# Kernel tuning notes

Hardware: AMD Instinct MI355X
Metric: run time of the kernel (lower is better)

## Reference

```python
import jax, jax.numpy as jnp
import numpy as np

B, T, D, NH, C = 64, 256, 768, 12, 7
DH = D // NH

def setup_inputs() -> dict:
    key = jax.random.key(0)
    ks = jax.random.split(key, 8)
    s = 0.02
    H = jax.random.normal(ks[0], (B, T, D), jnp.float32)
    num_turns = jax.random.randint(ks[1], (B,), 1, T + 1)  # >=1 real turn each
    Wq = jax.random.normal(ks[2], (D, D), jnp.float32) * s
    Wk = jax.random.normal(ks[3], (D, D), jnp.float32) * s
    Wv = jax.random.normal(ks[4], (D, D), jnp.float32) * s
    Wo = jax.random.normal(ks[5], (D, D), jnp.float32) * s
    Wc = jax.random.normal(ks[6], (2 * D, C), jnp.float32) * s
    bq = jnp.zeros((D,), jnp.float32); bk = jnp.zeros((D,), jnp.float32)
    bv = jnp.zeros((D,), jnp.float32); bo = jnp.zeros((D,), jnp.float32)
    bc = jnp.zeros((C,), jnp.float32)
    return dict(H=H, Wq=Wq, bq=bq, Wk=Wk, bk=bk, Wv=Wv, bv=bv, Wo=Wo, bo=bo,
                Wc=Wc, bc=bc, num_turns=num_turns)

def reference(H, Wq, bq, Wk, bk, Wv, bv, Wo, bo, Wc, bc, num_turns):
    # Vectorized form of the per-(dialogue, turn) python loop:
    # turn t attends (multi-head) over strictly-earlier real turns.
    q = (H @ Wq + bq).reshape(B, T, NH, DH)
    k = (H @ Wk + bk).reshape(B, T, NH, DH)
    v = (H @ Wv + bv).reshape(B, T, NH, DH)
    scores = jnp.einsum('bqhd,bkhd->bhqk', q, k) / np.sqrt(DH).astype(np.float32)
    tq = jnp.arange(T)
    # strict causal (key < query) AND key is a real (non-padding) turn
    mask = (tq[None, :, None] > tq[None, None, :]) & (tq[None, None, :] < num_turns[:, None, None])  # [B,T,T]
    scores = jnp.where(mask[:, None], scores, -1e30)
    attn = jax.nn.softmax(scores, axis=-1)
    row_valid = mask.any(-1)  # [B,T]; False for t=0 (and beyond padding prefix logic)
    attn = jnp.where(row_valid[:, None, :, None], attn, 0.0)
    ctx = jnp.einsum('bhqk,bkhd->bqhd', attn, v).reshape(B, T, D)
    c = ctx @ Wo + bo
    # t==0: original sets c_t = exact zeros (no out-proj bias) -> zero full rows
    c = jnp.where(row_valid[:, :, None], c, 0.0)
    z = jnp.concatenate([H, c], axis=-1)          # [B,T,2D]
    all_logits = z @ Wc + bc                       # [B,T,C]
    final_logits = all_logits[jnp.arange(B), num_turns - 1]  # [B,C]
    return all_logits, final_logits
```

## Files before the change

kernel.cpp:

```cpp
#include <hip/hip_runtime.h>
#include <hip/hip_bf16.h>

#define B_  64
#define T_  256
#define D_  768
#define NH_ 12
#define DH_ 64
#define C_  7
#define QS_ 2304

using f32x4  = __attribute__((ext_vector_type(4))) float;
using bf16x8 = __attribute__((ext_vector_type(8))) __bf16;
using u16x8  = __attribute__((ext_vector_type(8))) unsigned short;
using u16x4  = __attribute__((ext_vector_type(4))) unsigned short;
using s16x4  = __attribute__((ext_vector_type(4))) short;

#if defined(__has_builtin)
#if __has_builtin(__builtin_amdgcn_mfma_f32_16x16x16bf16_1k)
#define HAS_MFMA16 1
#endif
#endif

static __device__ inline unsigned short f2bf(float f) {
    union { float f; unsigned u; } c; c.f = f;
    unsigned u = c.u;
    return (unsigned short)((u + 0x7fffu + ((u >> 16) & 1u)) >> 16);
}

#define ASYNC16(gp, lp) __builtin_amdgcn_global_load_lds(                      \
    (const __attribute__((address_space(1))) unsigned int*)(gp),               \
    (__attribute__((address_space(3))) unsigned int*)(lp), 16, 0, 0)

#define PRO_CONV 6144
#define PRO_TR   1728
#define PRO_BIAS 9
#define PRO_WF   13
#define PRO_ALL  (PRO_CONV + PRO_TR + PRO_BIAS + PRO_WF)

__global__ __launch_bounds__(256) void prologue(
    const float* __restrict__ H, unsigned short* __restrict__ Hb,
    const float* __restrict__ Wq, const float* __restrict__ Wk,
    const float* __restrict__ Wv,
    unsigned short* __restrict__ Wqkvt,
    const float* __restrict__ bq, const float* __restrict__ bk,
    const float* __restrict__ bv, float* __restrict__ bqkv,
    const float* __restrict__ Wo, const float* __restrict__ Wc,
    const float* __restrict__ bo,
    float* __restrict__ Wf, float* __restrict__ boc)
{
    __shared__ float tile[32][33];
    __shared__ float wcs[D_ * C_];
    const int blk = blockIdx.x;
    const int tid = threadIdx.x;

    if (blk < PRO_CONV) {
        const int i = (blk * 256 + tid) * 8;
        float4 f0 = *(const float4*)(H + i);
        float4 f1 = *(const float4*)(H + i + 4);
        u16x8 u;
        u[0] = f2bf(f0.x); u[1] = f2bf(f0.y); u[2] = f2bf(f0.z); u[3] = f2bf(f0.w);
        u[4] = f2bf(f1.x); u[5] = f2bf(f1.y); u[6] = f2bf(f1.z); u[7] = f2bf(f1.w);
        *(uint4*)(Hb + i) = __builtin_bit_cast(uint4, u);
    } else if (blk < PRO_CONV + PRO_TR) {
        const int tb = blk - PRO_CONV;
        const int z = tb / 576;
        const int rem = tb - z * 576;
        const int bx = (rem % 24) * 32;
        const int by = (rem / 24) * 32;
        const size_t wsz = (size_t)D_ * D_;
        const float* W = (z == 0) ? Wq : (z == 1) ? Wk : Wv;
        unsigned short* Wt = Wqkvt + (size_t)z * wsz;
        const int tx = tid & 31;
        const int ty = tid >> 5;
#pragma unroll
        for (int i = ty; i < 32; i += 8)
            tile[i][tx] = W[(size_t)(by + i) * D_ + bx + tx];
        __syncthreads();
#pragma unroll
        for (int i = ty; i < 32; i += 8)
            Wt[(size_t)(bx + i) * D_ + by + tx] = f2bf(tile[tx][i]);
    } else if (blk < PRO_CONV + PRO_TR + PRO_BIAS) {
        const int i = (blk - PRO_CONV - PRO_TR) * 256 + tid;
        if (i < D_)          bqkv[i] = bq[i];
        else if (i < 2 * D_) bqkv[i] = bk[i - D_];
        else if (i < 3 * D_) bqkv[i] = bv[i - 2 * D_];
    } else {
        const int fb = blk - (PRO_CONV + PRO_TR + PRO_BIAS);
        for (int i = tid; i < D_ * C_; i += 256)
            wcs[i] = Wc[(size_t)D_ * C_ + i];
        __syncthreads();
        if (fb < 12) {
            const int dl = tid >> 2;
            const int ks = tid & 3;
            const int d  = fb * 64 + dl;
            const float* wrow = Wo + (size_t)d * D_;
            float a[C_] = {};
            for (int e = ks * 192; e < ks * 192 + 192; ++e) {
                const float w = wrow[e];
#pragma unroll
                for (int c = 0; c < C_; ++c) a[c] += w * wcs[e * C_ + c];
            }
#pragma unroll
            for (int c = 0; c < C_; ++c) {
                a[c] += __shfl_xor(a[c], 1, 64);
                a[c] += __shfl_xor(a[c], 2, 64);
            }
            if (ks == 0) {
#pragma unroll
                for (int c = 0; c < C_; ++c) Wf[d * C_ + c] = a[c];
            }
        } else if (tid < C_) {
            float a = 0.f;
            for (int e = 0; e < D_; ++e) a += bo[e] * wcs[e * C_ + tid];
            boc[tid] = a;
        }
    }
}

#define QBM 128
#define QBN 128
#define QBK 64
#define KQ  768
#define NKT 12

#define BAR   do { __builtin_amdgcn_s_barrier();                               \
                   __builtin_amdgcn_sched_barrier(0); } while (0)
#define VMW(n) do { asm volatile("s_waitcnt vmcnt(" #n ")" ::: "memory");      \
                    __builtin_amdgcn_sched_barrier(0); } while (0)

__global__ __launch_bounds__(256, 2) void gemm_qkv_db(
    const unsigned short* __restrict__ A,
    const unsigned short* __restrict__ Bt,
    const float* __restrict__ bias,
    unsigned short* __restrict__ qkvb,
    unsigned short* __restrict__ Vt,
    const int* __restrict__ num_turns)
{
    __shared__ unsigned short As[2][QBM * QBK];
    __shared__ unsigned short Bs[2][QBN * QBK];

    const int tid = threadIdx.x;
    const int wv  = tid >> 6;
    const int ln  = tid & 63;
    const int hi  = ln >> 4;
    const int lo  = ln & 15;
    const int wm  = (wv & 1) * 64;
    const int wn  = (wv >> 1) * 64;

    const int L   = blockIdx.y * gridDim.x + blockIdx.x;
    const int wg  = (L & 7) * 288 + (L >> 3);
    const int my  = wg / 18;
    const int nx  = wg - my * 18;

    const int row0 = my * QBM;
    const int col0 = nx * QBN;

    if (col0 >= D_ && (row0 & (T_ - 1)) != 0) {
        if (num_turns[row0 >> 8] <= 128) return;
    }

    const int s0 = tid >> 3;
    const int ch = (tid & 7) ^ (s0 & 7);
    const unsigned short* a0 = A  + (size_t)(row0 + s0) * KQ + ch * 8;
    const unsigned short* b0 = Bt + (size_t)(col0 + s0) * KQ + ch * 8;

#define STG(t, q) do {                                                         \
    _Pragma("unroll") for (int c = 0; c < 4; ++c) {                            \
        ASYNC16(a0 + (size_t)(t) * QBK + (size_t)c * 32 * KQ,                  \
                &As[q][c * 2048 + wv * 512]);                                  \
        ASYNC16(b0 + (size_t)(t) * QBK + (size_t)c * 32 * KQ,                  \
                &Bs[q][c * 2048 + wv * 512]);                                  \
    }                                                                          \
} while (0)

    const int fcs[2] = { (0 * 4 + hi) ^ (lo & 7), (1 * 4 + hi) ^ (lo & 7) };

    f32x4 acc[4][4] = {};

#define TILE(t, q, qn) do {                                                    \
    if ((t) + 1 < NKT) { STG((t) + 1, qn); VMW(8); }                           \
    else               { VMW(0); }                                             \
    BAR;                                                                       \
    _Pragma("unroll") for (int s = 0; s < 2; ++s) {                            \
        const int fc = fcs[s];                                                 \
        bf16x8 af[4], bfr[4];                                                  \
        _Pragma("unroll") for (int i = 0; i < 4; ++i)                          \
            af[i] = *(const bf16x8*)&As[q][(wm + i * 16 + lo) * QBK + fc * 8]; \
        _Pragma("unroll") for (int j = 0; j < 4; ++j)                          \
            bfr[j] = *(const bf16x8*)&Bs[q][(wn + j * 16 + lo) * QBK + fc * 8];\
        __builtin_amdgcn_s_setprio(1);                                         \
        _Pragma("unroll") for (int i = 0; i < 4; ++i)                          \
        _Pragma("unroll") for (int j = 0; j < 4; ++j)                          \
            acc[i][j] = __builtin_amdgcn_mfma_f32_16x16x32_bf16(               \
                af[i], bfr[j], acc[i][j], 0, 0, 0);                            \
        __builtin_amdgcn_s_setprio(0);                                         \
    }                                                                          \
    BAR;                                                                       \
} while (0)

    STG(0, 0);
#pragma unroll
    for (int g = 0; g < NKT; g += 2) {
        TILE(g + 0, 0, 1);
        TILE(g + 1, 1, 0);
    }
#undef STG
#undef TILE

    const int bidx = row0 >> 8;
    const int t0   = row0 & (T_ - 1);
    if (col0 >= 1536) {
#pragma unroll
        for (int j = 0; j < 4; ++j) {
            const int dcol = (col0 - 1536) + wn + j * 16 + lo;
            const float bcol = bias[col0 + wn + j * 16 + lo];
            unsigned short* vrow =
                Vt + ((size_t)(bidx * NH_ + (dcol >> 6)) * DH_ + (dcol & 63)) * T_ + t0;
#pragma unroll
            for (int i = 0; i < 4; ++i) {
                u16x4 pk;
#pragma unroll
                for (int r = 0; r < 4; ++r) pk[r] = f2bf(acc[i][j][r] + bcol);
                *(u16x4*)(vrow + wm + i * 16 + hi * 4) = pk;
            }
        }
        return;
    }
#pragma unroll
    for (int j = 0; j < 4; ++j) {
        const int col = col0 + wn + j * 16 + lo;
        const float bcol = bias[col];
#pragma unroll
        for (int i = 0; i < 4; ++i) {
#pragma unroll
            for (int r = 0; r < 4; ++r) {
                const int row = row0 + wm + i * 16 + hi * 4 + r;
                qkvb[(size_t)row * QS_ + col] = f2bf(acc[i][j][r] + bcol);
            }
        }
    }
}

#if HAS_MFMA16
__global__ __launch_bounds__(512) void attn_fused(
    const unsigned short* __restrict__ qkv, const unsigned short* __restrict__ Vt,
    const int* __restrict__ num_turns, unsigned short* __restrict__ ctx)
{
    __shared__ unsigned short Klds[256 * 64];
    __shared__ unsigned short Vlds[64 * 256];

    const int bh = blockIdx.x;
    const int b = bh / NH_;
    const int h = bh - b * NH_;
    const int tid = threadIdx.x;
    const int wave = tid >> 6;
    const int lane = tid & 63;
    const int hi = lane >> 4;
    const int lo = lane & 15;
    const int lo7 = lo & 7;

    const int nt = num_turns[b];
    const int kend16 = (min(254, nt - 1) >> 4) + 1;
    const int vst = (kend16 <= 8) ? 128 : 256;

    const unsigned short* qb  = qkv + (size_t)(b * T_) * QS_ + h * DH_;
    const unsigned short* kb  = qb + D_;
    const unsigned short* vtb = Vt + (size_t)bh * DH_ * T_;

    {
        const int nkc = kend16 * 128;
        for (int q = tid; q < nkc; q += 512) {
            const int row = q >> 3;
            const int c   = q & 7;
            const int sl  = c ^ (row & 7);
            uint4 v = *(const uint4*)(kb + (size_t)row * QS_ + c * 8);
            *(uint4*)&Klds[row * 64 + sl * 8] = v;
        }
    }
    if (vst == 256) {
        for (int q = tid; q < 2048; q += 512) {
            const int d  = q >> 5;
            const int c  = q & 31;
            const int sl = c ^ (d & 7);
            uint4 v = *(const uint4*)(vtb + (size_t)d * T_ + c * 8);
            *(uint4*)&Vlds[d * 256 + sl * 8] = v;
        }
    } else {
        for (int q = tid; q < 1024; q += 512) {
            const int d  = q >> 4;
            const int c  = q & 15;
            const int sl = c ^ (d & 7);
            uint4 v = *(const uint4*)(vtb + (size_t)d * T_ + c * 8);
            *(uint4*)&Vlds[d * 128 + sl * 8] = v;
        }
    }

    bf16x8 aqs[2][2];
#pragma unroll
    for (int i = 0; i < 2; ++i) {
        const int m0 = (i ? (15 - wave) : wave) * 16;
#pragma unroll
        for (int ks = 0; ks < 2; ++ks)
            aqs[i][ks] = *(const bf16x8*)(qb + (size_t)(m0 + lo) * QS_ + ks * 32 + hi * 8);
    }

    __syncthreads();

#pragma unroll
    for (int i = 0; i < 2; ++i) {
        const int tq = i ? (15 - wave) : wave;
        const int m0 = tq * 16;
        const int qrow = m0 + lo;
        const int kmax  = min(m0 + 14, nt - 1);
        const int ktmax = kmax >> 4;

        f32x4 s[16] = {};
#pragma unroll
        for (int kt = 0; kt < 16; ++kt) {
            if (kt <= ktmax) {
#pragma unroll
                for (int ks = 0; ks < 2; ++ks) {
                    bf16x8 kf = *(const bf16x8*)&Klds[(kt * 16 + lo) * 64
                                                     + ((ks * 4 + hi) ^ lo7) * 8];
                    s[kt] = __builtin_amdgcn_mfma_f32_16x16x32_bf16(kf, aqs[i][ks], s[kt], 0, 0, 0);
                }
            }
        }

        float lsum = 0.f;
        s16x4 pf[16];
#pragma unroll
        for (int kt = 0; kt < 16; ++kt) {
            if (kt <= ktmax) {
#pragma unroll
                for (int r = 0; r < 4; ++r) {
                    const int key = kt * 16 + hi * 4 + r;
                    const bool valid = (key < qrow) && (key < nt);
                    const float p = valid ? __expf(s[kt][r] * 0.125f) : 0.f;
                    lsum += p;
                    pf[kt][r] = (short)f2bf(p);
                }
            }
        }

        f32x4 o[4] = {};
#pragma unroll
        for (int kt = 0; kt < 16; ++kt) {
            if (kt <= ktmax) {
#pragma unroll
                for (int nd = 0; nd < 4; ++nd) {
                    const int cidx = (kt * 2 + (hi >> 1)) ^ lo7;
                    s16x4 bv = *(const s16x4*)&Vlds[(nd * 16 + lo) * vst
                                                    + cidx * 8 + (hi & 1) * 4];
                    o[nd] = __builtin_amdgcn_mfma_f32_16x16x16bf16_1k(pf[kt], bv, o[nd], 0, 0, 0);
                }
            }
        }

        lsum += __shfl_xor(lsum, 16, 64);
        lsum += __shfl_xor(lsum, 32, 64);
        float linv[4];
#pragma unroll
        for (int r = 0; r < 4; ++r) {
            const float lq = __shfl(lsum, hi * 4 + r, 64);
            linv[r] = (lq > 0.f) ? (1.f / lq) : 0.f;
        }

#pragma unroll
        for (int nd = 0; nd < 4; ++nd) {
#pragma unroll
            for (int r = 0; r < 4; ++r) {
                ctx[((size_t)(b * T_ + m0 + hi * 4 + r)) * D_ + h * DH_ + nd * 16 + lo]
                    = f2bf(o[nd][r] * linv[r]);
            }
        }
    }
}
#else
__global__ __launch_bounds__(512) void attn_fused(
    const unsigned short* __restrict__ qkv, const unsigned short* __restrict__ Vt,
    const int* __restrict__ num_turns, unsigned short* __restrict__ ctx)
{
    __shared__ unsigned short Plds[8][16 * 264];

    const int bh = blockIdx.x;
    const int b = bh / NH_;
    const int h = bh - b * NH_;
    const int tid = threadIdx.x;
    const int wave = tid >> 6;
    const int lane = tid & 63;
    const int hi = lane >> 4;
    const int lo = lane & 15;

    const int nt = num_turns[b];
    const unsigned short* qb = qkv + (size_t)(b * T_) * QS_ + h * DH_;
    const unsigned short* kb = qb + D_;
    const unsigned short* vtb = Vt + (size_t)bh * DH_ * T_;

    for (int ii = 0; ii < 2; ++ii) {
        const int m0 = (ii ? (15 - wave) : wave) * 16;
        const int kmax = min(m0 + 14, nt - 1);
        const int n0hi = (kmax >> 4) | 1;
        const int nks  = (kmax >> 5) + 1;

        bf16x8 aq[2];
#pragma unroll
        for (int ks = 0; ks < 2; ++ks)
            aq[ks] = *(const bf16x8*)(qb + (size_t)(m0 + lo) * QS_ + ks * 32 + hi * 8);

        f32x4 s[16] = {};
#pragma unroll
        for (int n0 = 0; n0 < 16; ++n0) {
            if (n0 <= n0hi) {
#pragma unroll
                for (int ks = 0; ks < 2; ++ks) {
                    bf16x8 bk = *(const bf16x8*)(kb + (size_t)(n0 * 16 + lo) * QS_ + ks * 32 + hi * 8);
                    s[n0] = __builtin_amdgcn_mfma_f32_16x16x32_bf16(aq[ks], bk, s[n0], 0, 0, 0);
                }
            }
        }

#pragma unroll
        for (int r = 0; r < 4; ++r) {
            const int qrow = m0 + hi * 4 + r;
            float mr = -1e30f;
#pragma unroll
            for (int n0 = 0; n0 < 16; ++n0) {
                if (n0 <= n0hi) {
                    int key = n0 * 16 + lo;
                    bool valid = (key < qrow) && (key < nt);
                    float se = valid ? s[n0][r] * 0.125f : -1e30f;
                    s[n0][r] = se;
                    mr = fmaxf(mr, se);
                }
            }
#pragma unroll
            for (int off = 1; off < 16; off <<= 1) mr = fmaxf(mr, __shfl_xor(mr, off, 64));

            float lr = 0.f;
#pragma unroll
            for (int n0 = 0; n0 < 16; ++n0) {
                if (n0 <= n0hi) {
                    float se = s[n0][r];
                    float pv = (se > -5e29f) ? __expf(se - mr) : 0.f;
                    s[n0][r] = pv;
                    lr += pv;
                }
            }
#pragma unroll
            for (int off = 1; off < 16; off <<= 1) lr += __shfl_xor(lr, off, 64);

            float inv = (lr > 0.f) ? (1.f / lr) : 0.f;
#pragma unroll
            for (int n0 = 0; n0 < 16; ++n0) {
                if (n0 <= n0hi) {
                    Plds[wave][(hi * 4 + r) * 264 + n0 * 16 + lo] = f2bf(s[n0][r] * inv);
                }
            }
        }

        f32x4 o[4] = {};
#pragma unroll
        for (int ks = 0; ks < 8; ++ks) {
            if (ks < nks) {
                const unsigned short* lp = &Plds[wave][lo * 264 + ks * 32 + hi * 8];
                bf16x8 ap = __builtin_bit_cast(bf16x8, *(const uint4*)lp);
#pragma unroll
                for (int nd = 0; nd < 4; ++nd) {
                    bf16x8 bvf = *(const bf16x8*)(vtb + (size_t)(nd * 16 + lo) * T_ + ks * 32 + hi * 8);
                    o[nd] = __builtin_amdgcn_mfma_f32_16x16x32_bf16(ap, bvf, o[nd], 0, 0, 0);
                }
            }
        }

#pragma unroll
        for (int nd = 0; nd < 4; ++nd) {
#pragma unroll
            for (int r = 0; r < 4; ++r) {
                ctx[((size_t)(b * T_ + m0 + hi * 4 + r)) * D_ + h * DH_ + nd * 16 + lo]
                    = f2bf(o[nd][r]);
            }
        }
    }
}
#endif

#define WCP 1544

__global__ __launch_bounds__(256) void logits_mfma(
    const unsigned short* __restrict__ Hb, const unsigned short* __restrict__ ctxb,
    const float* __restrict__ Wc, const float* __restrict__ Wf,
    const float* __restrict__ bc, const float* __restrict__ boc,
    const int* __restrict__ num_turns, float* __restrict__ out)
{
    __shared__ unsigned short sW[16 * WCP];

    const int tid = threadIdx.x;
    const int wave = tid >> 6;
    const int lane = tid & 63;
    const int hi = lane >> 4;
    const int lo = lane & 15;

    for (int i = tid; i < 16 * 1536; i += 256) {
        int n = i & 15, kk = i >> 4;
        float val = 0.f;
        if (n < C_)
            val = (kk < D_) ? Wc[(size_t)kk * C_ + n] : Wf[(kk - D_) * C_ + n];
        sW[n * WCP + kk] = f2bf(val);
    }
    __syncthreads();

    const int m0 = blockIdx.x * 64 + wave * 16;
    const unsigned short* hrow = Hb   + (size_t)(m0 + lo) * D_;
    const unsigned short* crow = ctxb + (size_t)(m0 + lo) * D_;

    f32x4 acc = {};
#pragma unroll
    for (int kt = 0; kt < 24; ++kt) {
        bf16x8 a = *(const bf16x8*)(hrow + kt * 32 + hi * 8);
        bf16x8 w = *(const bf16x8*)&sW[lo * WCP + kt * 32 + hi * 8];
        acc = __builtin_amdgcn_mfma_f32_16x16x32_bf16(a, w, acc, 0, 0, 0);
    }
#pragma unroll
    for (int kt = 0; kt < 24; ++kt) {
        bf16x8 a = *(const bf16x8*)(crow + kt * 32 + hi * 8);
        bf16x8 w = *(const bf16x8*)&sW[lo * WCP + (768 + kt * 32) + hi * 8];
        acc = __builtin_amdgcn_mfma_f32_16x16x32_bf16(a, w, acc, 0, 0, 0);
    }

    if (lo < C_) {
        const float b0 = bc[lo];
        const float b1 = boc[lo];
#pragma unroll
        for (int r = 0; r < 4; ++r) {
            const int row = m0 + hi * 4 + r;
            const int t = row & (T_ - 1);
            const float tot = acc[r] + b0 + ((t != 0) ? b1 : 0.f);
            out[(size_t)row * C_ + lo] = tot;
            const int b = row >> 8;
            if (t == num_turns[b] - 1)
                out[(size_t)B_ * T_ * C_ + (size_t)b * C_ + lo] = tot;
        }
    }
}

extern "C" void kernel_launch(void* const* d_in, const int* in_sizes, int n_in,
                              void* d_out, int out_size, void* d_ws, size_t ws_size,
                              hipStream_t stream)
{
    const float* H  = (const float*)d_in[0];
    const float* Wq = (const float*)d_in[1];
    const float* bq = (const float*)d_in[2];
    const float* Wk = (const float*)d_in[3];
    const float* bk = (const float*)d_in[4];
    const float* Wv = (const float*)d_in[5];
    const float* bv = (const float*)d_in[6];
    const float* Wo = (const float*)d_in[7];
    const float* bo = (const float*)d_in[8];
    const float* Wc = (const float*)d_in[9];
    const float* bc = (const float*)d_in[10];
    const int* num_turns = (const int*)d_in[11];
    float* out = (float*)d_out;

    const int M = B_ * T_;
    const size_t per = (size_t)M * D_;
    const size_t wsz = (size_t)D_ * D_;

    unsigned short* ws16 = (unsigned short*)d_ws;
    unsigned short* Hb    = ws16;
    unsigned short* Wqkvt = Hb + per;
    unsigned short* qkvb  = Wqkvt + 3 * wsz;
    unsigned short* ctxb  = qkvb + (size_t)M * QS_;
    unsigned short* Vtb   = ctxb + per;
    float* bqkv = (float*)(Vtb + per);
    float* Wf   = bqkv + QS_;
    float* boc  = Wf + (size_t)D_ * C_;

    prologue<<<PRO_ALL, 256, 0, stream>>>(H, Hb, Wq, Wk, Wv, Wqkvt,
                                          bq, bk, bv, bqkv,
                                          Wo, Wc, bo, Wf, boc);

    dim3 qkvGrid(18, 128);
    gemm_qkv_db<<<qkvGrid, 256, 0, stream>>>(Hb, Wqkvt, bqkv, qkvb,
                                             Vtb, num_turns);

    attn_fused<<<B_ * NH_, 512, 0, stream>>>(qkvb, Vtb, num_turns, ctxb);

    logits_mfma<<<M / 64, 256, 0, stream>>>(Hb, ctxb, Wc, Wf, bc, boc,
                                            num_turns, out);
}
```

Measured before the change: 262.5 us.

## Fuse folded Wo·Wc projection into attention epilogue, emit per-head partial logits

The attention kernel no longer writes the bf16 context tensor. Each block multiplies its head's output by the matching slice of the folded Wo·Wc matrix, reduces across lanes with shuffles, and writes per-head partial logits (7 values, padded to 8) to a small fp32 buffer. The logits kernel then only runs the H·Wc MFMA over 768 instead of 1536 and adds the 12 per-head partials. This removes the context write and re-read and halves the logits GEMM, at the cost of extra shuffle reductions and scattered 4-byte stores in the attention epilogue.

```diff
diff --git a/kernel.cpp b/kernel.cpp
--- a/kernel.cpp
+++ b/kernel.cpp
@@ -8,6 +8,7 @@
 #define DH_ 64
 #define C_  7
 #define QS_ 2304
+#define HPS 96
 
 using f32x4  = __attribute__((ext_vector_type(4))) float;
 using bf16x8 = __attribute__((ext_vector_type(8))) __bf16;
@@ -244,10 +245,12 @@
 #if HAS_MFMA16
 __global__ __launch_bounds__(512) void attn_fused(
     const unsigned short* __restrict__ qkv, const unsigned short* __restrict__ Vt,
-    const int* __restrict__ num_turns, unsigned short* __restrict__ ctx)
+    const float* __restrict__ Wf, const int* __restrict__ num_turns,
+    float* __restrict__ hp)
 {
     __shared__ unsigned short Klds[256 * 64];
     __shared__ unsigned short Vlds[64 * 256];
+    __shared__ float Wlds[64 * 8];
 
     const int bh = blockIdx.x;
     const int b = bh / NH_;
@@ -268,6 +271,10 @@
     const unsigned short* vtb = Vt + (size_t)bh * DH_ * T_;
 
     {
+        const int dd = tid >> 3, c = tid & 7;
+        Wlds[dd * 8 + (c ^ (dd & 7))] = (c < C_) ? Wf[(h * 64 + dd) * C_ + c] : 0.f;
+    }
+    {
         const int nkc = kend16 * 128;
         for (int q = tid; q < nkc; q += 512) {
             const int row = q >> 3;
@@ -367,11 +374,20 @@
         }
 
 #pragma unroll
-        for (int nd = 0; nd < 4; ++nd) {
-#pragma unroll
-            for (int r = 0; r < 4; ++r) {
-                ctx[((size_t)(b * T_ + m0 + hi * 4 + r)) * D_ + h * DH_ + nd * 16 + lo]
-                    = f2bf(o[nd][r] * linv[r]);
+        for (int r = 0; r < 4; ++r) {
+            const size_t row = (size_t)(b * T_ + m0 + hi * 4 + r);
+#pragma unroll
+            for (int c = 0; c < C_; ++c) {
+                float s2 = 0.f;
+#pragma unroll
+                for (int nd = 0; nd < 4; ++nd)
+                    s2 += o[nd][r] * Wlds[(nd * 16 + lo) * 8 + (c ^ lo7)];
+                s2 *= linv[r];
+                s2 += __shfl_xor(s2, 1, 64);
+                s2 += __shfl_xor(s2, 2, 64);
+                s2 += __shfl_xor(s2, 4, 64);
+                s2 += __shfl_xor(s2, 8, 64);
+                if (lo == c) hp[row * HPS + h * 8 + c] = s2;
             }
         }
     }
@@ -379,9 +395,11 @@
 #else
 __global__ __launch_bounds__(512) void attn_fused(
     const unsigned short* __restrict__ qkv, const unsigned short* __restrict__ Vt,
-    const int* __restrict__ num_turns, unsigned short* __restrict__ ctx)
+    const float* __restrict__ Wf, const int* __restrict__ num_turns,
+    float* __restrict__ hp)
 {
     __shared__ unsigned short Plds[8][16 * 264];
+    __shared__ float Wlds[64 * 8];
 
     const int bh = blockIdx.x;
     const int b = bh / NH_;
@@ -391,11 +409,18 @@
     const int lane = tid & 63;
     const int hi = lane >> 4;
     const int lo = lane & 15;
+    const int lo7 = lo & 7;
 
     const int nt = num_turns[b];
     const unsigned short* qb = qkv + (size_t)(b * T_) * QS_ + h * DH_;
     const unsigned short* kb = qb + D_;
     const unsigned short* vtb = Vt + (size_t)bh * DH_ * T_;
+
+    {
+        const int dd = tid >> 3, c = tid & 7;
+        Wlds[dd * 8 + (c ^ (dd & 7))] = (c < C_) ? Wf[(h * 64 + dd) * C_ + c] : 0.f;
+    }
+    __syncthreads();
 
     for (int ii = 0; ii < 2; ++ii) {
         const int m0 = (ii ? (15 - wave) : wave) * 16;
@@ -474,26 +499,34 @@
         }
 
 #pragma unroll
-        for (int nd = 0; nd < 4; ++nd) {
-#pragma unroll
-            for (int r = 0; r < 4; ++r) {
-                ctx[((size_t)(b * T_ + m0 + hi * 4 + r)) * D_ + h * DH_ + nd * 16 + lo]
-                    = f2bf(o[nd][r]);
+        for (int r = 0; r < 4; ++r) {
+            const size_t row = (size_t)(b * T_ + m0 + hi * 4 + r);
+#pragma unroll
+            for (int c = 0; c < C_; ++c) {
+                float s2 = 0.f;
+#pragma unroll
+                for (int nd = 0; nd < 4; ++nd)
+                    s2 += o[nd][r] * Wlds[(nd * 16 + lo) * 8 + (c ^ lo7)];
+                s2 += __shfl_xor(s2, 1, 64);
+                s2 += __shfl_xor(s2, 2, 64);
+                s2 += __shfl_xor(s2, 4, 64);
+                s2 += __shfl_xor(s2, 8, 64);
+                if (lo == c) hp[row * HPS + h * 8 + c] = s2;
             }
         }
     }
 }
 #endif
 
-#define WCP 1544
+#define WCP2 776
 
 __global__ __launch_bounds__(256) void logits_mfma(
-    const unsigned short* __restrict__ Hb, const unsigned short* __restrict__ ctxb,
-    const float* __restrict__ Wc, const float* __restrict__ Wf,
-    const float* __restrict__ bc, const float* __restrict__ boc,
-    const int* __restrict__ num_turns, float* __restrict__ out)
+    const unsigned short* __restrict__ Hb, const float* __restrict__ hp,
+    const float* __restrict__ Wc, const float* __restrict__ bc,
+    const float* __restrict__ boc, const int* __restrict__ num_turns,
+    float* __restrict__ out)
 {
-    __shared__ unsigned short sW[16 * WCP];
+    __shared__ unsigned short sW[16 * WCP2];
 
     const int tid = threadIdx.x;
     const int wave = tid >> 6;
@@ -501,30 +534,21 @@
     const int hi = lane >> 4;
     const int lo = lane & 15;
 
-    for (int i = tid; i < 16 * 1536; i += 256) {
+    for (int i = tid; i < 16 * 768; i += 256) {
         int n = i & 15, kk = i >> 4;
-        float val = 0.f;
-        if (n < C_)
-            val = (kk < D_) ? Wc[(size_t)kk * C_ + n] : Wf[(kk - D_) * C_ + n];
-        sW[n * WCP + kk] = f2bf(val);
+        float val = (n < C_) ? Wc[(size_t)kk * C_ + n] : 0.f;
+        sW[n * WCP2 + kk] = f2bf(val);
     }
     __syncthreads();
 
     const int m0 = blockIdx.x * 64 + wave * 16;
-    const unsigned short* hrow = Hb   + (size_t)(m0 + lo) * D_;
-    const unsigned short* crow = ctxb + (size_t)(m0 + lo) * D_;
+    const unsigned short* hrow = Hb + (size_t)(m0 + lo) * D_;
 
     f32x4 acc = {};
 #pragma unroll
     for (int kt = 0; kt < 24; ++kt) {
         bf16x8 a = *(const bf16x8*)(hrow + kt * 32 + hi * 8);
-        bf16x8 w = *(const bf16x8*)&sW[lo * WCP + kt * 32 + hi * 8];
-        acc = __builtin_amdgcn_mfma_f32_16x16x32_bf16(a, w, acc, 0, 0, 0);
-    }
-#pragma unroll
-    for (int kt = 0; kt < 24; ++kt) {
-        bf16x8 a = *(const bf16x8*)(crow + kt * 32 + hi * 8);
-        bf16x8 w = *(const bf16x8*)&sW[lo * WCP + (768 + kt * 32) + hi * 8];
+        bf16x8 w = *(const bf16x8*)&sW[lo * WCP2 + kt * 32 + hi * 8];
         acc = __builtin_amdgcn_mfma_f32_16x16x32_bf16(a, w, acc, 0, 0, 0);
     }
 
@@ -535,7 +559,11 @@
         for (int r = 0; r < 4; ++r) {
             const int row = m0 + hi * 4 + r;
             const int t = row & (T_ - 1);
-            const float tot = acc[r] + b0 + ((t != 0) ? b1 : 0.f);
+            float hs = 0.f;
+#pragma unroll
+            for (int hh = 0; hh < NH_; ++hh)
+                hs += hp[(size_t)row * HPS + hh * 8 + lo];
+            const float tot = acc[r] + b0 + ((t != 0) ? b1 : 0.f) + hs;
             out[(size_t)row * C_ + lo] = tot;
             const int b = row >> 8;
             if (t == num_turns[b] - 1)
@@ -570,8 +598,8 @@
     unsigned short* Hb    = ws16;
     unsigned short* Wqkvt = Hb + per;
     unsigned short* qkvb  = Wqkvt + 3 * wsz;
-    unsigned short* ctxb  = qkvb + (size_t)M * QS_;
-    unsigned short* Vtb   = ctxb + per;
+    float*          hp    = (float*)(qkvb + (size_t)M * QS_);
+    unsigned short* Vtb   = (unsigned short*)(hp + (size_t)M * HPS);
     float* bqkv = (float*)(Vtb + per);
     float* Wf   = bqkv + QS_;
     float* boc  = Wf + (size_t)D_ * C_;
@@ -584,8 +612,8 @@
     gemm_qkv_db<<<qkvGrid, 256, 0, stream>>>(Hb, Wqkvt, bqkv, qkvb,
                                              Vtb, num_turns);
 
-    attn_fused<<<B_ * NH_, 512, 0, stream>>>(qkvb, Vtb, num_turns, ctxb);
-
-    logits_mfma<<<M / 64, 256, 0, stream>>>(Hb, ctxb, Wc, Wf, bc, boc,
+    attn_fused<<<B_ * NH_, 512, 0, stream>>>(qkvb, Vtb, Wf, num_turns, hp);
+
+    logits_mfma<<<M / 64, 256, 0, stream>>>(Hb, hp, Wc, bc, boc,
                                             num_turns, out);
 }
```

After: 267.6 us. No clear change (+1.9%).

## Use async global-to-LDS loads for K/V staging and reorder prologue blocks

Applied to the files above, without the earlier changes.

The attention kernel now stages K and V tiles into LDS with global_load_lds direct transfers instead of loading through registers. Each lane's source column is pre-swizzled so the destination layout matches the old XOR-swizzled layout. A vmcnt(0) wait is added before the barrier. The prologue block order is also changed so the small, long-running Wf fold and bias blocks dispatch first, ahead of the conversion and transpose blocks, which shortens the tail.

```diff
diff --git a/kernel.cpp b/kernel.cpp
--- a/kernel.cpp
+++ b/kernel.cpp
@@ -31,11 +31,11 @@
     (const __attribute__((address_space(1))) unsigned int*)(gp),               \
     (__attribute__((address_space(3))) unsigned int*)(lp), 16, 0, 0)
 
+#define PRO_WF   13
+#define PRO_BIAS 9
+#define PRO_TR   1728
 #define PRO_CONV 6144
-#define PRO_TR   1728
-#define PRO_BIAS 9
-#define PRO_WF   13
-#define PRO_ALL  (PRO_CONV + PRO_TR + PRO_BIAS + PRO_WF)
+#define PRO_ALL  (PRO_WF + PRO_BIAS + PRO_TR + PRO_CONV)
 
 __global__ __launch_bounds__(256) void prologue(
     const float* __restrict__ H, unsigned short* __restrict__ Hb,
@@ -53,39 +53,8 @@
     const int blk = blockIdx.x;
     const int tid = threadIdx.x;
 
-    if (blk < PRO_CONV) {
-        const int i = (blk * 256 + tid) * 8;
-        float4 f0 = *(const float4*)(H + i);
-        float4 f1 = *(const float4*)(H + i + 4);
-        u16x8 u;
-        u[0] = f2bf(f0.x); u[1] = f2bf(f0.y); u[2] = f2bf(f0.z); u[3] = f2bf(f0.w);
-        u[4] = f2bf(f1.x); u[5] = f2bf(f1.y); u[6] = f2bf(f1.z); u[7] = f2bf(f1.w);
-        *(uint4*)(Hb + i) = __builtin_bit_cast(uint4, u);
-    } else if (blk < PRO_CONV + PRO_TR) {
-        const int tb = blk - PRO_CONV;
-        const int z = tb / 576;
-        const int rem = tb - z * 576;
-        const int bx = (rem % 24) * 32;
-        const int by = (rem / 24) * 32;
-        const size_t wsz = (size_t)D_ * D_;
-        const float* W = (z == 0) ? Wq : (z == 1) ? Wk : Wv;
-        unsigned short* Wt = Wqkvt + (size_t)z * wsz;
-        const int tx = tid & 31;
-        const int ty = tid >> 5;
-#pragma unroll
-        for (int i = ty; i < 32; i += 8)
-            tile[i][tx] = W[(size_t)(by + i) * D_ + bx + tx];
-        __syncthreads();
-#pragma unroll
-        for (int i = ty; i < 32; i += 8)
-            Wt[(size_t)(bx + i) * D_ + by + tx] = f2bf(tile[tx][i]);
-    } else if (blk < PRO_CONV + PRO_TR + PRO_BIAS) {
-        const int i = (blk - PRO_CONV - PRO_TR) * 256 + tid;
-        if (i < D_)          bqkv[i] = bq[i];
-        else if (i < 2 * D_) bqkv[i] = bk[i - D_];
-        else if (i < 3 * D_) bqkv[i] = bv[i - 2 * D_];
-    } else {
-        const int fb = blk - (PRO_CONV + PRO_TR + PRO_BIAS);
+    if (blk < PRO_WF) {
+        const int fb = blk;
         for (int i = tid; i < D_ * C_; i += 256)
             wcs[i] = Wc[(size_t)D_ * C_ + i];
         __syncthreads();
@@ -114,6 +83,37 @@
             for (int e = 0; e < D_; ++e) a += bo[e] * wcs[e * C_ + tid];
             boc[tid] = a;
         }
+    } else if (blk < PRO_WF + PRO_BIAS) {
+        const int i = (blk - PRO_WF) * 256 + tid;
+        if (i < D_)          bqkv[i] = bq[i];
+        else if (i < 2 * D_) bqkv[i] = bk[i - D_];
+        else if (i < 3 * D_) bqkv[i] = bv[i - 2 * D_];
+    } else if (blk < PRO_WF + PRO_BIAS + PRO_TR) {
+        const int tb = blk - PRO_WF - PRO_BIAS;
+        const int z = tb / 576;
+        const int rem = tb - z * 576;
+        const int bx = (rem % 24) * 32;
+        const int by = (rem / 24) * 32;
+        const size_t wsz = (size_t)D_ * D_;
+        const float* W = (z == 0) ? Wq : (z == 1) ? Wk : Wv;
+        unsigned short* Wt = Wqkvt + (size_t)z * wsz;
+        const int tx = tid & 31;
+        const int ty = tid >> 5;
+#pragma unroll
+        for (int i = ty; i < 32; i += 8)
+            tile[i][tx] = W[(size_t)(by + i) * D_ + bx + tx];
+        __syncthreads();
+#pragma unroll
+        for (int i = ty; i < 32; i += 8)
+            Wt[(size_t)(bx + i) * D_ + by + tx] = f2bf(tile[tx][i]);
+    } else {
+        const int i = ((blk - PRO_WF - PRO_BIAS - PRO_TR) * 256 + tid) * 8;
+        float4 f0 = *(const float4*)(H + i);
+        float4 f1 = *(const float4*)(H + i + 4);
+        u16x8 u;
+        u[0] = f2bf(f0.x); u[1] = f2bf(f0.y); u[2] = f2bf(f0.z); u[3] = f2bf(f0.w);
+        u[4] = f2bf(f1.x); u[5] = f2bf(f1.y); u[6] = f2bf(f1.z); u[7] = f2bf(f1.w);
+        *(uint4*)(Hb + i) = __builtin_bit_cast(uint4, u);
     }
 }
 
@@ -268,30 +268,24 @@
     const unsigned short* vtb = Vt + (size_t)bh * DH_ * T_;
 
     {
-        const int nkc = kend16 * 128;
-        for (int q = tid; q < nkc; q += 512) {
-            const int row = q >> 3;
-            const int c   = q & 7;
-            const int sl  = c ^ (row & 7);
-            uint4 v = *(const uint4*)(kb + (size_t)row * QS_ + c * 8);
-            *(uint4*)&Klds[row * 64 + sl * 8] = v;
+        const int nr = kend16 * 2;
+        for (int rd = wave; rd < nr; rd += 8) {
+            const int row = rd * 8 + (lane >> 3);
+            const int c   = (lane & 7) ^ (row & 7);
+            ASYNC16(kb + (size_t)row * QS_ + c * 8, &Klds[rd * 512]);
         }
     }
     if (vst == 256) {
-        for (int q = tid; q < 2048; q += 512) {
-            const int d  = q >> 5;
-            const int c  = q & 31;
-            const int sl = c ^ (d & 7);
-            uint4 v = *(const uint4*)(vtb + (size_t)d * T_ + c * 8);
-            *(uint4*)&Vlds[d * 256 + sl * 8] = v;
+        for (int rd = wave; rd < 32; rd += 8) {
+            const int d = rd * 2 + (lane >> 5);
+            const int c = (lane & 31) ^ (d & 7);
+            ASYNC16(vtb + (size_t)d * T_ + c * 8, &Vlds[rd * 512]);
         }
     } else {
-        for (int q = tid; q < 1024; q += 512) {
-            const int d  = q >> 4;
-            const int c  = q & 15;
-            const int sl = c ^ (d & 7);
-            uint4 v = *(const uint4*)(vtb + (size_t)d * T_ + c * 8);
-            *(uint4*)&Vlds[d * 128 + sl * 8] = v;
+        for (int rd = wave; rd < 16; rd += 8) {
+            const int d = rd * 4 + (lane >> 4);
+            const int c = (lane & 15) ^ (d & 7);
+            ASYNC16(vtb + (size_t)d * T_ + c * 8, &Vlds[rd * 512]);
         }
     }
 
@@ -304,6 +298,7 @@
             aqs[i][ks] = *(const bf16x8*)(qb + (size_t)(m0 + lo) * QS_ + ks * 32 + hi * 8);
     }
 
+    asm volatile("s_waitcnt vmcnt(0)" ::: "memory");
     __syncthreads();
 
 #pragma unroll
```

After: 252.4 us. 1.04x faster.
